# Optimization experiments

Measured on AMD Instinct MI355X. Metric: run time of the kernel, lower is better.

Reference implementation:

```python
import jax, jax.numpy as jnp
import numpy as np

B = 32768
IN_DIM = 256
HIDDEN = 256  # max(64, in_dim)
E = 8         # num_size_classes
K = 5         # num_depth_classes


def setup_inputs() -> dict:
    key = jax.random.key(0)
    ks = jax.random.split(key, 6)
    x = jax.random.normal(ks[0], (B, IN_DIM), dtype=jnp.float32)
    size_idx = jax.random.randint(ks[1], (B,), 0, E, dtype=jnp.int32)
    s1 = 1.0 / np.sqrt(IN_DIM)
    s2 = 1.0 / np.sqrt(HIDDEN)
    W1 = jax.random.uniform(ks[2], (E, IN_DIM, HIDDEN), jnp.float32, -s1, s1)
    b1 = jax.random.uniform(ks[3], (E, HIDDEN), jnp.float32, -s1, s1)
    W2 = jax.random.uniform(ks[4], (E, HIDDEN, K - 1), jnp.float32, -s2, s2)
    b2 = jax.random.uniform(ks[5], (E, K - 1), jnp.float32, -s2, s2)
    return {"x": x, "size_idx": size_idx, "W1": W1, "b1": b1, "W2": W2, "b2": b2}


def ordinal_logits_to_probs(logits):
    # logits: [B, K-1] cumulative ordinal logits -> [B, K] class probabilities
    q = jax.nn.sigmoid(logits)
    probs = jnp.concatenate(
        [1.0 - q[:, :1], q[:, :-1] - q[:, 1:], q[:, -1:]], axis=1)
    probs = jnp.clip(probs, 1e-8)
    return probs / jnp.clip(jnp.sum(probs, axis=1, keepdims=True), 1e-8)


def reference(x, size_idx, W1, b1, W2, b2):
    # Hard expert dispatch: each sample routed to expert[size_idx].
    # Equivalent to torch's boolean-mask loop (every row has a valid expert).
    # Compute all experts densely (grouped GEMM), then select per sample.
    h = jax.nn.relu(jnp.einsum('bi,eih->beh', x, W1) + b1)       # [B,E,H]
    logits_all = jnp.einsum('beh,ehk->bek', h, W2) + b2           # [B,E,K-1]
    idx = size_idx.astype(jnp.int32)[:, None, None]               # [B,1,1]
    logits = jnp.take_along_axis(logits_all, idx, axis=1)[:, 0]   # [B,K-1]
    probs = ordinal_logits_to_probs(logits)
    return logits, probs
```

## Files before the change

kernel.cpp:

```cpp
#include <hip/hip_runtime.h>
#include <stdint.h>
#include <math.h>

#define B_N   32768
#define INDIM 256
#define HID   256
#define NE    8
#define KM1   4
#define KCLS  5
#define BM    64
#define NBLK  ((B_N + NE * BM) / BM)

typedef __bf16 bf16x8 __attribute__((ext_vector_type(8)));
typedef float  f32x4  __attribute__((ext_vector_type(4)));
typedef unsigned short u16x8 __attribute__((ext_vector_type(8)));

__device__ __forceinline__ unsigned short f2bf(float f) {
    union { float f; unsigned u; } v; v.f = f;
    unsigned r = v.u + 0x7FFFu + ((v.u >> 16) & 1u);
    return (unsigned short)(r >> 16);
}
__device__ __forceinline__ float bf2f(unsigned short b) {
    union { unsigned u; float f; } v; v.u = ((unsigned)b) << 16;
    return v.f;
}
__device__ __forceinline__ int SWZ(int r, int c) {
    return c ^ ((r & 7) << 2) ^ ((r >> 3) & 3);
}

__global__ __launch_bounds__(256) void k_w1t(const float* __restrict__ W1,
                                             const int* __restrict__ sidx,
                                             unsigned short* __restrict__ w1p,
                                             int* __restrict__ part) {
    __shared__ float tile[64][65];
    __shared__ int wc[4][NE];
    int t    = threadIdx.x;
    int b    = blockIdx.x;
    int lane = t & 63;
    int wave = t >> 6;

    int i = b * 256 + t;
    int es = sidx[i];
    #pragma unroll
    for (int t2 = 0; t2 < NE; ++t2) {
        unsigned long long m = __ballot(es == t2);
        if (lane == t2) wc[wave][t2] = (int)__popcll(m);
    }

    int e  = b >> 4;
    int ti = (b >> 2) & 3;
    int th = b & 3;
    const float* src = W1 + (((size_t)e * INDIM) + (size_t)ti * 64) * HID + th * 64;
    int col = t & 63;
    int r0  = (t >> 6) * 16;
    #pragma unroll
    for (int rr = 0; rr < 16; ++rr)
        tile[r0 + rr][col] = src[(size_t)(r0 + rr) * HID + col];
    __syncthreads();

    if (t < NE) part[b * NE + t] = wc[0][t] + wc[1][t] + wc[2][t] + wc[3][t];

    int u = t >> 6;
    #pragma unroll
    for (int ks2 = 0; ks2 < 2; ++ks2) {
        int ks = ti * 2 + ks2;
        int nb = th * 4 + u;
        u16x8 v;
        #pragma unroll
        for (int j = 0; j < 8; ++j)
            v[j] = f2bf(tile[ks2 * 32 + (lane >> 4) * 8 + j][u * 16 + (lane & 15)]);
        *(u16x8*)&w1p[((((size_t)e * 8 + ks) * 16 + nb) * 64 + lane) * 8] = v;
    }
}

__global__ __launch_bounds__(256) void k_scatter(const int* __restrict__ sidx,
                                                 const int* __restrict__ part,
                                                 int* __restrict__ perm,
                                                 int* __restrict__ meta) {
    __shared__ int pp[128][NE];
    __shared__ int pre8[NE], tot8[NE];
    __shared__ int wc[4][NE];
    int t    = threadIdx.x;
    int b    = blockIdx.x;
    int lane = t & 63;
    int wave = t >> 6;

    if (t < 128) {
        #pragma unroll
        for (int e2 = 0; e2 < NE; ++e2) pp[t][e2] = part[t * NE + e2];
    }
    int i = b * 256 + t;
    int e = sidx[i];
    int posw = 0;
    #pragma unroll
    for (int t2 = 0; t2 < NE; ++t2) {
        unsigned long long m = __ballot(e == t2);
        if (e == t2) posw = (int)__popcll(m & ((1ull << lane) - 1ull));
        if (lane == t2) wc[wave][t2] = (int)__popcll(m);
    }
    __syncthreads();
    if (t < NE) {
        int s = 0, a = 0;
        for (int b2 = 0; b2 < 128; ++b2) {
            int v = pp[b2][t];
            if (b2 < b) s += v;
            a += v;
        }
        pre8[t] = s; tot8[t] = a;
        meta[t] = a;
    }
    __syncthreads();
    int off = 0;
    #pragma unroll
    for (int t2 = 0; t2 < NE; ++t2)
        off += (t2 < e) ? (((tot8[t2] + 63) >> 6) << 6) : 0;
    int wsum = 0;
    #pragma unroll
    for (int w2 = 0; w2 < 4; ++w2)
        wsum += (w2 < wave) ? wc[w2][e] : 0;
    perm[off + pre8[e] + wsum + posw] = i;
}

__global__ __launch_bounds__(256, 3) void k_main(
    const float* __restrict__ x,  const float* __restrict__ b1,
    const float* __restrict__ W2, const float* __restrict__ b2,
    const unsigned short* __restrict__ w1p,
    const int* __restrict__ perm, const int* __restrict__ meta,
    float* __restrict__ out)
{
    __shared__ unsigned short xs[BM * 256];
    __shared__ float w2s[1040];

    int base = blockIdx.x * BM;
    int e = 0, segstart = 0, segcnt = 0, acc_off = 0;
    #pragma unroll
    for (int t = 0; t < NE; ++t) {
        int c  = meta[t];
        int st = acc_off;
        acc_off += ((c + 63) >> 6) << 6;
        if (base >= st) { e = t; segstart = st; segcnt = c; }
    }
    if (base >= acc_off) return;
    int segend = segstart + segcnt;

    int tid  = threadIdx.x;
    int lane = tid & 63;
    int wave = tid >> 6;
    int r15  = lane & 15;
    int hi   = lane >> 4;

    {
        int row  = tid & 63;
        int q    = tid >> 6;
        int prow = base + row;
        int smp  = (prow < segend) ? perm[prow] : -1;
        const float* xr = x + (size_t)(smp < 0 ? 0 : smp) * INDIM + q * 64;
        #pragma unroll
        for (int cc = 0; cc < 8; ++cc) {
            int csw = SWZ(row, q * 8 + cc);
            u16x8 v = {0, 0, 0, 0, 0, 0, 0, 0};
            if (smp >= 0) {
                const f32x4* p4 = (const f32x4*)(xr + cc * 8);
                f32x4 a0 = p4[0], a1 = p4[1];
                v[0] = f2bf(a0[0]); v[1] = f2bf(a0[1]); v[2] = f2bf(a0[2]); v[3] = f2bf(a0[3]);
                v[4] = f2bf(a1[0]); v[5] = f2bf(a1[1]); v[6] = f2bf(a1[2]); v[7] = f2bf(a1[3]);
            }
            *(u16x8*)&xs[row * 256 + (csw << 3)] = v;
        }
    }
    {
        const float* w2e = W2 + (size_t)e * HID * KM1;
        f32x4 wv = *(const f32x4*)(w2e + (size_t)tid * 4);
        *(f32x4*)&w2s[tid * 4 + (tid >> 6) * 4] = wv;
    }
    __syncthreads();

    const unsigned short* w1pe = w1p + (size_t)e * (8 * 16 * 64 * 8);
    auto loadB = [&](int ks, int ni) -> bf16x8 {
        return *(const bf16x8*)&w1pe[(((ks * 16 + wave * 4 + ni) * 64) + lane) * 8];
    };

    f32x4 acc[4][4];
    #pragma unroll
    for (int mi = 0; mi < 4; ++mi)
        #pragma unroll
        for (int ni = 0; ni < 4; ++ni) {
            f32x4 z = {0.f, 0.f, 0.f, 0.f};
            acc[mi][ni] = z;
        }

    bf16x8 bcur[4];
    #pragma unroll
    for (int ni = 0; ni < 4; ++ni) bcur[ni] = loadB(0, ni);

    #pragma unroll
    for (int ks = 0; ks < 8; ++ks) {
        bf16x8 bnext[4];
        if (ks < 7) {
            #pragma unroll
            for (int ni = 0; ni < 4; ++ni) bnext[ni] = loadB(ks + 1, ni);
        }
        bf16x8 af[4];
        #pragma unroll
        for (int mi = 0; mi < 4; ++mi) {
            int r = mi * 16 + r15;
            af[mi] = *(const bf16x8*)&xs[r * 256 + (SWZ(r, ks * 4 + hi) << 3)];
        }
        #pragma unroll
        for (int mi = 0; mi < 4; ++mi)
            #pragma unroll
            for (int ni = 0; ni < 4; ++ni)
                acc[mi][ni] = __builtin_amdgcn_mfma_f32_16x16x32_bf16(
                    af[mi], bcur[ni], acc[mi][ni], 0, 0, 0);
        if (ks < 7) {
            #pragma unroll
            for (int ni = 0; ni < 4; ++ni) bcur[ni] = bnext[ni];
        }
    }
    __syncthreads();

    float b1v[4];
    #pragma unroll
    for (int ni = 0; ni < 4; ++ni)
        b1v[ni] = b1[e * HID + wave * 64 + ni * 16 + r15];
    #pragma unroll
    for (int mi = 0; mi < 4; ++mi) {
        #pragma unroll
        for (int ni = 0; ni < 4; ++ni) {
            int colg  = wave * 64 + ni * 16 + r15;
            int chunk = colg >> 3;
            #pragma unroll
            for (int j = 0; j < 4; ++j) {
                int rowg = mi * 16 + hi * 4 + j;
                float h = fmaxf(acc[mi][ni][j] + b1v[ni], 0.f);
                xs[rowg * 256 + (SWZ(rowg, chunk) << 3) + (colg & 7)] = f2bf(h);
            }
        }
    }
    __syncthreads();

    int row2 = tid >> 2;
    int q2   = tid & 3;
    f32x4 lac = {0.f, 0.f, 0.f, 0.f};
    #pragma unroll
    for (int s = 0; s < 8; ++s) {
        int c = q2 * 8 + s;
        u16x8 hv = *(const u16x8*)&xs[row2 * 256 + (SWZ(row2, c) << 3)];
        #pragma unroll
        for (int j = 0; j < 8; ++j) {
            int k = c * 8 + j;
            float hf = bf2f(hv[j]);
            const f32x4 wv = *(const f32x4*)&w2s[k * 4 + (k >> 6) * 4];
            lac[0] += hf * wv[0]; lac[1] += hf * wv[1];
            lac[2] += hf * wv[2]; lac[3] += hf * wv[3];
        }
    }
    #pragma unroll
    for (int c4 = 0; c4 < 4; ++c4) {
        lac[c4] += __shfl_xor(lac[c4], 1, 4);
        lac[c4] += __shfl_xor(lac[c4], 2, 4);
    }

    if (base + row2 < segend) {
        int smp = perm[base + row2];
        const float* b2e = b2 + e * KM1;
        float l0 = lac[0] + b2e[0], l1 = lac[1] + b2e[1];
        float l2 = lac[2] + b2e[2], l3 = lac[3] + b2e[3];
        float q0 = 1.f / (1.f + expf(-l0)), q1 = 1.f / (1.f + expf(-l1));
        float q2v = 1.f / (1.f + expf(-l2)), q3 = 1.f / (1.f + expf(-l3));
        float p0 = fmaxf(1.f - q0, 1e-8f), p1 = fmaxf(q0 - q1, 1e-8f);
        float p2 = fmaxf(q1 - q2v, 1e-8f), p3 = fmaxf(q2v - q3, 1e-8f);
        float p4 = fmaxf(q3, 1e-8f);
        float inv = 1.f / (p0 + p1 + p2 + p3 + p4);
        float myl = (q2 & 1) ? ((q2 & 2) ? l3 : l1) : ((q2 & 2) ? l2 : l0);
        float myp = (q2 & 1) ? ((q2 & 2) ? p3 : p1) : ((q2 & 2) ? p2 : p0);
        out[(size_t)smp * KM1 + q2] = myl;
        float* probs = out + (size_t)B_N * KM1;
        probs[(size_t)smp * KCLS + q2] = myp * inv;
        if (q2 == 3) probs[(size_t)smp * KCLS + 4] = p4 * inv;
    }
}

extern "C" void kernel_launch(void* const* d_in, const int* in_sizes, int n_in,
                              void* d_out, int out_size, void* d_ws, size_t ws_size,
                              hipStream_t stream) {
    const float* x   = (const float*)d_in[0];
    const int*   sid = (const int*)d_in[1];
    const float* W1  = (const float*)d_in[2];
    const float* b1  = (const float*)d_in[3];
    const float* W2  = (const float*)d_in[4];
    const float* b2  = (const float*)d_in[5];
    float* out = (float*)d_out;

    char* ws = (char*)d_ws;
    unsigned short* w1p = (unsigned short*)ws;
    int* perm = (int*)(ws + 1048576);
    int* part = (int*)(ws + 1048576 + 133120);
    int* meta = (int*)(ws + 1048576 + 133120 + 4096);

    k_w1t    <<<dim3(128),  dim3(256), 0, stream>>>(W1, sid, w1p, part);
    k_scatter<<<dim3(128),  dim3(256), 0, stream>>>(sid, part, perm, meta);
    k_main   <<<dim3(NBLK), dim3(256), 0, stream>>>(x, b1, W2, b2, w1p, perm, meta, out);
}
```

Baseline: 33.83 us.

## Halve row tile to 32, raise occupancy, hoist B prefetch above x staging

```diff
diff --git a/kernel.cpp b/kernel.cpp
--- a/kernel.cpp
+++ b/kernel.cpp
@@ -8,7 +8,7 @@
 #define NE    8
 #define KM1   4
 #define KCLS  5
-#define BM    64
+#define BM    32
 #define NBLK  ((B_N + NE * BM) / BM)
 
 typedef __bf16 bf16x8 __attribute__((ext_vector_type(8)));
@@ -24,9 +24,7 @@
     union { unsigned u; float f; } v; v.u = ((unsigned)b) << 16;
     return v.f;
 }
-__device__ __forceinline__ int SWZ(int r, int c) {
-    return c ^ ((r & 7) << 2) ^ ((r >> 3) & 3);
-}
+__device__ __forceinline__ int SWZ(int r, int c) { return c ^ (r & 7); }
 
 __global__ __launch_bounds__(256) void k_w1t(const float* __restrict__ W1,
                                              const int* __restrict__ sidx,
@@ -113,7 +111,7 @@
     int off = 0;
     #pragma unroll
     for (int t2 = 0; t2 < NE; ++t2)
-        off += (t2 < e) ? (((tot8[t2] + 63) >> 6) << 6) : 0;
+        off += (t2 < e) ? (((tot8[t2] + BM - 1) / BM) * BM) : 0;
     int wsum = 0;
     #pragma unroll
     for (int w2 = 0; w2 < 4; ++w2)
@@ -121,7 +119,7 @@
     perm[off + pre8[e] + wsum + posw] = i;
 }
 
-__global__ __launch_bounds__(256, 3) void k_main(
+__global__ __launch_bounds__(256, 4) void k_main(
     const float* __restrict__ x,  const float* __restrict__ b1,
     const float* __restrict__ W2, const float* __restrict__ b2,
     const unsigned short* __restrict__ w1p,
@@ -137,7 +135,7 @@
     for (int t = 0; t < NE; ++t) {
         int c  = meta[t];
         int st = acc_off;
-        acc_off += ((c + 63) >> 6) << 6;
+        acc_off += ((c + BM - 1) / BM) * BM;
         if (base >= st) { e = t; segstart = st; segcnt = c; }
     }
     if (base >= acc_off) return;
@@ -149,15 +147,22 @@
     int r15  = lane & 15;
     int hi   = lane >> 4;
 
+    const unsigned short* w1pe = w1p + (size_t)e * (8 * 16 * 64 * 8);
+    auto loadB = [&](int ks, int ni) -> bf16x8 {
+        return *(const bf16x8*)&w1pe[(((ks * 16 + wave * 4 + ni) * 64) + lane) * 8];
+    };
+    bf16x8 bcur[4];
+    #pragma unroll
+    for (int ni = 0; ni < 4; ++ni) bcur[ni] = loadB(0, ni);
+
+    int row = tid >> 3;
+    int q   = tid & 7;
+    int smp = (base + row < segend) ? perm[base + row] : -1;
     {
-        int row  = tid & 63;
-        int q    = tid >> 6;
-        int prow = base + row;
-        int smp  = (prow < segend) ? perm[prow] : -1;
-        const float* xr = x + (size_t)(smp < 0 ? 0 : smp) * INDIM + q * 64;
-        #pragma unroll
-        for (int cc = 0; cc < 8; ++cc) {
-            int csw = SWZ(row, q * 8 + cc);
+        const float* xr = x + (size_t)(smp < 0 ? 0 : smp) * INDIM + q * 32;
+        #pragma unroll
+        for (int cc = 0; cc < 4; ++cc) {
+            int csw = SWZ(row, q * 4 + cc);
             u16x8 v = {0, 0, 0, 0, 0, 0, 0, 0};
             if (smp >= 0) {
                 const f32x4* p4 = (const f32x4*)(xr + cc * 8);
@@ -175,23 +180,14 @@
     }
     __syncthreads();
 
-    const unsigned short* w1pe = w1p + (size_t)e * (8 * 16 * 64 * 8);
-    auto loadB = [&](int ks, int ni) -> bf16x8 {
-        return *(const bf16x8*)&w1pe[(((ks * 16 + wave * 4 + ni) * 64) + lane) * 8];
-    };
-
-    f32x4 acc[4][4];
-    #pragma unroll
-    for (int mi = 0; mi < 4; ++mi)
+    f32x4 acc[2][4];
+    #pragma unroll
+    for (int mi = 0; mi < 2; ++mi)
         #pragma unroll
         for (int ni = 0; ni < 4; ++ni) {
             f32x4 z = {0.f, 0.f, 0.f, 0.f};
             acc[mi][ni] = z;
         }
-
-    bf16x8 bcur[4];
-    #pragma unroll
-    for (int ni = 0; ni < 4; ++ni) bcur[ni] = loadB(0, ni);
 
     #pragma unroll
     for (int ks = 0; ks < 8; ++ks) {
@@ -200,14 +196,14 @@
             #pragma unroll
             for (int ni = 0; ni < 4; ++ni) bnext[ni] = loadB(ks + 1, ni);
         }
-        bf16x8 af[4];
-        #pragma unroll
-        for (int mi = 0; mi < 4; ++mi) {
+        bf16x8 af[2];
+        #pragma unroll
+        for (int mi = 0; mi < 2; ++mi) {
             int r = mi * 16 + r15;
             af[mi] = *(const bf16x8*)&xs[r * 256 + (SWZ(r, ks * 4 + hi) << 3)];
         }
         #pragma unroll
-        for (int mi = 0; mi < 4; ++mi)
+        for (int mi = 0; mi < 2; ++mi)
             #pragma unroll
             for (int ni = 0; ni < 4; ++ni)
                 acc[mi][ni] = __builtin_amdgcn_mfma_f32_16x16x32_bf16(
@@ -224,7 +220,7 @@
     for (int ni = 0; ni < 4; ++ni)
         b1v[ni] = b1[e * HID + wave * 64 + ni * 16 + r15];
     #pragma unroll
-    for (int mi = 0; mi < 4; ++mi) {
+    for (int mi = 0; mi < 2; ++mi) {
         #pragma unroll
         for (int ni = 0; ni < 4; ++ni) {
             int colg  = wave * 64 + ni * 16 + r15;
@@ -239,13 +235,11 @@
     }
     __syncthreads();
 
-    int row2 = tid >> 2;
-    int q2   = tid & 3;
     f32x4 lac = {0.f, 0.f, 0.f, 0.f};
     #pragma unroll
-    for (int s = 0; s < 8; ++s) {
-        int c = q2 * 8 + s;
-        u16x8 hv = *(const u16x8*)&xs[row2 * 256 + (SWZ(row2, c) << 3)];
+    for (int s = 0; s < 4; ++s) {
+        int c = q * 4 + ((s + q) & 3);
+        u16x8 hv = *(const u16x8*)&xs[row * 256 + (SWZ(row, c) << 3)];
         #pragma unroll
         for (int j = 0; j < 8; ++j) {
             int k = c * 8 + j;
@@ -257,12 +251,12 @@
     }
     #pragma unroll
     for (int c4 = 0; c4 < 4; ++c4) {
-        lac[c4] += __shfl_xor(lac[c4], 1, 4);
-        lac[c4] += __shfl_xor(lac[c4], 2, 4);
-    }
-
-    if (base + row2 < segend) {
-        int smp = perm[base + row2];
+        lac[c4] += __shfl_xor(lac[c4], 1, 8);
+        lac[c4] += __shfl_xor(lac[c4], 2, 8);
+        lac[c4] += __shfl_xor(lac[c4], 4, 8);
+    }
+
+    if (smp >= 0 && q < 5) {
         const float* b2e = b2 + e * KM1;
         float l0 = lac[0] + b2e[0], l1 = lac[1] + b2e[1];
         float l2 = lac[2] + b2e[2], l3 = lac[3] + b2e[3];
@@ -272,12 +266,15 @@
         float p2 = fmaxf(q1 - q2v, 1e-8f), p3 = fmaxf(q2v - q3, 1e-8f);
         float p4 = fmaxf(q3, 1e-8f);
         float inv = 1.f / (p0 + p1 + p2 + p3 + p4);
-        float myl = (q2 & 1) ? ((q2 & 2) ? l3 : l1) : ((q2 & 2) ? l2 : l0);
-        float myp = (q2 & 1) ? ((q2 & 2) ? p3 : p1) : ((q2 & 2) ? p2 : p0);
-        out[(size_t)smp * KM1 + q2] = myl;
         float* probs = out + (size_t)B_N * KM1;
-        probs[(size_t)smp * KCLS + q2] = myp * inv;
-        if (q2 == 3) probs[(size_t)smp * KCLS + 4] = p4 * inv;
+        if (q < 4) {
+            float myl = (q & 1) ? ((q & 2) ? l3 : l1) : ((q & 2) ? l2 : l0);
+            float myp = (q & 1) ? ((q & 2) ? p3 : p1) : ((q & 2) ? p2 : p0);
+            out[(size_t)smp * KM1 + q] = myl;
+            probs[(size_t)smp * KCLS + q] = myp * inv;
+        } else {
+            probs[(size_t)smp * KCLS + 4] = p4 * inv;
+        }
     }
 }
 
@@ -295,8 +292,8 @@
     char* ws = (char*)d_ws;
     unsigned short* w1p = (unsigned short*)ws;
     int* perm = (int*)(ws + 1048576);
-    int* part = (int*)(ws + 1048576 + 133120);
-    int* meta = (int*)(ws + 1048576 + 133120 + 4096);
+    int* part = (int*)(ws + 1048576 + 135168);
+    int* meta = (int*)(ws + 1048576 + 135168 + 4096);
 
     k_w1t    <<<dim3(128),  dim3(256), 0, stream>>>(W1, sid, w1p, part);
     k_scatter<<<dim3(128),  dim3(256), 0, stream>>>(sid, part, perm, meta);
```

Result: no change. 34.27 us (+1.3%).

## Fuse prep kernels, pre-scatter bf16 x into expert-bucketed buffer, DMA into LDS

Applied to the files above, without the earlier changes.

```diff
diff --git a/kernel.cpp b/kernel.cpp
--- a/kernel.cpp
+++ b/kernel.cpp
@@ -9,7 +9,9 @@
 #define KM1   4
 #define KCLS  5
 #define BM    64
-#define NBLK  ((B_N + NE * BM) / BM)
+#define CAP   8192
+#define TPE   (CAP / BM)
+#define NBLK  (NE * TPE)
 
 typedef __bf16 bf16x8 __attribute__((ext_vector_type(8)));
 typedef float  f32x4  __attribute__((ext_vector_type(4)));
@@ -24,124 +26,132 @@
     union { unsigned u; float f; } v; v.u = ((unsigned)b) << 16;
     return v.f;
 }
-__device__ __forceinline__ int SWZ(int r, int c) {
-    return c ^ ((r & 7) << 2) ^ ((r >> 3) & 3);
-}
-
-__global__ __launch_bounds__(256) void k_w1t(const float* __restrict__ W1,
-                                             const int* __restrict__ sidx,
-                                             unsigned short* __restrict__ w1p,
-                                             int* __restrict__ part) {
+__device__ __forceinline__ int SWZ(int r, int c) { return c ^ (r & 7); }
+
+__device__ __forceinline__ void gload_lds16(const void* g, void* l) {
+    __builtin_amdgcn_global_load_lds(
+        (__attribute__((address_space(1))) unsigned int*)(g),
+        (__attribute__((address_space(3))) unsigned int*)(l),
+        16, 0, 0);
+}
+
+__global__ __launch_bounds__(256) void k_prep(
+    const float* __restrict__ W1, const float* __restrict__ x,
+    const int* __restrict__ sidx,
+    unsigned short* __restrict__ w1p, unsigned short* __restrict__ xb,
+    int* __restrict__ perm, int* __restrict__ meta)
+{
     __shared__ float tile[64][65];
-    __shared__ int wc[4][NE];
+    __shared__ int wsum[4][NE];
+    __shared__ int gcnt[2][NE];
+    __shared__ int pcs[NE];
+    __shared__ int posbuf[128];
+
     int t    = threadIdx.x;
     int b    = blockIdx.x;
     int lane = t & 63;
     int wave = t >> 6;
 
-    int i = b * 256 + t;
-    int es = sidx[i];
-    #pragma unroll
-    for (int t2 = 0; t2 < NE; ++t2) {
-        unsigned long long m = __ballot(es == t2);
-        if (lane == t2) wc[wave][t2] = (int)__popcll(m);
-    }
-
-    int e  = b >> 4;
-    int ti = (b >> 2) & 3;
-    int th = b & 3;
-    const float* src = W1 + (((size_t)e * INDIM) + (size_t)ti * 64) * HID + th * 64;
-    int col = t & 63;
-    int r0  = (t >> 6) * 16;
-    #pragma unroll
-    for (int rr = 0; rr < 16; ++rr)
-        tile[r0 + rr][col] = src[(size_t)(r0 + rr) * HID + col];
-    __syncthreads();
-
-    if (t < NE) part[b * NE + t] = wc[0][t] + wc[1][t] + wc[2][t] + wc[3][t];
-
-    int u = t >> 6;
-    #pragma unroll
-    for (int ks2 = 0; ks2 < 2; ++ks2) {
-        int ks = ti * 2 + ks2;
-        int nb = th * 4 + u;
-        u16x8 v;
-        #pragma unroll
-        for (int j = 0; j < 8; ++j)
-            v[j] = f2bf(tile[ks2 * 32 + (lane >> 4) * 8 + j][u * 16 + (lane & 15)]);
-        *(u16x8*)&w1p[((((size_t)e * 8 + ks) * 16 + nb) * 64 + lane) * 8] = v;
-    }
-}
-
-__global__ __launch_bounds__(256) void k_scatter(const int* __restrict__ sidx,
-                                                 const int* __restrict__ part,
-                                                 int* __restrict__ perm,
-                                                 int* __restrict__ meta) {
-    __shared__ int pp[128][NE];
-    __shared__ int pre8[NE], tot8[NE];
-    __shared__ int wc[4][NE];
-    int t    = threadIdx.x;
-    int b    = blockIdx.x;
-    int lane = t & 63;
-    int wave = t >> 6;
-
+    if (b < 128) {
+        int e  = b >> 4, ti = (b >> 2) & 3, th = b & 3;
+        const float* src = W1 + (((size_t)e * INDIM) + (size_t)ti * 64) * HID + th * 64;
+        int col = t & 63, r0 = (t >> 6) * 16;
+        #pragma unroll
+        for (int rr = 0; rr < 16; ++rr)
+            tile[r0 + rr][col] = src[(size_t)(r0 + rr) * HID + col];
+    }
+
+    int cnt[NE] = {0, 0, 0, 0, 0, 0, 0, 0};
+    int nch = (b * 128) >> 6;
+    for (int j = wave; j < nch; j += 4) {
+        int v = sidx[j * 64 + lane];
+        #pragma unroll
+        for (int t2 = 0; t2 < NE; ++t2) {
+            unsigned long long m = __ballot(v == t2);
+            cnt[t2] += (int)__popcll(m);
+        }
+    }
+    if (lane == 0) {
+        #pragma unroll
+        for (int t2 = 0; t2 < NE; ++t2) wsum[wave][t2] = cnt[t2];
+    }
+    __syncthreads();
+    if (t < NE) pcs[t] = wsum[0][t] + wsum[1][t] + wsum[2][t] + wsum[3][t];
+
+    int e_own = 0, posw = 0;
     if (t < 128) {
-        #pragma unroll
-        for (int e2 = 0; e2 < NE; ++e2) pp[t][e2] = part[t * NE + e2];
-    }
-    int i = b * 256 + t;
-    int e = sidx[i];
-    int posw = 0;
-    #pragma unroll
-    for (int t2 = 0; t2 < NE; ++t2) {
-        unsigned long long m = __ballot(e == t2);
-        if (e == t2) posw = (int)__popcll(m & ((1ull << lane) - 1ull));
-        if (lane == t2) wc[wave][t2] = (int)__popcll(m);
-    }
-    __syncthreads();
-    if (t < NE) {
-        int s = 0, a = 0;
-        for (int b2 = 0; b2 < 128; ++b2) {
-            int v = pp[b2][t];
-            if (b2 < b) s += v;
-            a += v;
-        }
-        pre8[t] = s; tot8[t] = a;
-        meta[t] = a;
-    }
-    __syncthreads();
-    int off = 0;
-    #pragma unroll
-    for (int t2 = 0; t2 < NE; ++t2)
-        off += (t2 < e) ? (((tot8[t2] + 63) >> 6) << 6) : 0;
-    int wsum = 0;
-    #pragma unroll
-    for (int w2 = 0; w2 < 4; ++w2)
-        wsum += (w2 < wave) ? wc[w2][e] : 0;
-    perm[off + pre8[e] + wsum + posw] = i;
-}
-
-__global__ __launch_bounds__(256, 3) void k_main(
-    const float* __restrict__ x,  const float* __restrict__ b1,
-    const float* __restrict__ W2, const float* __restrict__ b2,
+        e_own = sidx[b * 128 + t];
+        #pragma unroll
+        for (int t2 = 0; t2 < NE; ++t2) {
+            unsigned long long m = __ballot(e_own == t2);
+            if (e_own == t2) posw = (int)__popcll(m & ((1ull << lane) - 1ull));
+            if (lane == t2) gcnt[wave][t2] = (int)__popcll(m);
+        }
+    }
+    __syncthreads();
+    if (t < 128) {
+        int grp  = (wave == 1) ? gcnt[0][e_own] : 0;
+        int rank = pcs[e_own] + grp + posw;
+        int pos  = e_own * CAP + rank;
+        posbuf[t] = pos;
+        perm[pos] = b * 128 + t;
+    }
+    if (b == 255 && t < NE) meta[t] = pcs[t] + gcnt[0][t] + gcnt[1][t];
+
+    if (b < 128) {
+        int e  = b >> 4, ti = (b >> 2) & 3, th = b & 3;
+        int u = t >> 6;
+        #pragma unroll
+        for (int ks2 = 0; ks2 < 2; ++ks2) {
+            int ks = ti * 2 + ks2, nb = th * 4 + u;
+            u16x8 v;
+            #pragma unroll
+            for (int j = 0; j < 8; ++j)
+                v[j] = f2bf(tile[ks2 * 32 + (lane >> 4) * 8 + j][u * 16 + (lane & 15)]);
+            *(u16x8*)&w1p[((((size_t)e * 8 + ks) * 16 + nb) * 64 + lane) * 8] = v;
+        }
+    }
+    __syncthreads();
+
+    {
+        int si  = t & 127, h = t >> 7;
+        int i   = b * 128 + si;
+        int pos = posbuf[si];
+        int r   = pos & (BM - 1);
+        const float* xr = x + (size_t)i * INDIM + h * 128;
+        unsigned short* dst = xb + (size_t)pos * 256;
+        #pragma unroll
+        for (int cc = 0; cc < 16; ++cc) {
+            int ch   = h * 16 + cc;
+            int slot = SWZ(r, ch);
+            f32x4 a0 = *(const f32x4*)(xr + cc * 8);
+            f32x4 a1 = *(const f32x4*)(xr + cc * 8 + 4);
+            u16x8 v;
+            v[0] = f2bf(a0[0]); v[1] = f2bf(a0[1]); v[2] = f2bf(a0[2]); v[3] = f2bf(a0[3]);
+            v[4] = f2bf(a1[0]); v[5] = f2bf(a1[1]); v[6] = f2bf(a1[2]); v[7] = f2bf(a1[3]);
+            *(u16x8*)&dst[slot * 8] = v;
+        }
+    }
+}
+
+__global__ __launch_bounds__(256, 4) void k_main(
+    const float* __restrict__ b1, const float* __restrict__ W2,
+    const float* __restrict__ b2,
     const unsigned short* __restrict__ w1p,
+    const unsigned short* __restrict__ xb,
     const int* __restrict__ perm, const int* __restrict__ meta,
     float* __restrict__ out)
 {
     __shared__ unsigned short xs[BM * 256];
     __shared__ float w2s[1040];
 
-    int base = blockIdx.x * BM;
-    int e = 0, segstart = 0, segcnt = 0, acc_off = 0;
-    #pragma unroll
-    for (int t = 0; t < NE; ++t) {
-        int c  = meta[t];
-        int st = acc_off;
-        acc_off += ((c + 63) >> 6) << 6;
-        if (base >= st) { e = t; segstart = st; segcnt = c; }
-    }
-    if (base >= acc_off) return;
-    int segend = segstart + segcnt;
+    int bid = (blockIdx.x & 7) * TPE + (blockIdx.x >> 3);
+    int e   = bid >> 7;
+    int tl  = bid & (TPE - 1);
+    int cnt = meta[e];
+    int rb  = tl * BM;
+    if (rb >= cnt) return;
+    int segc = cnt - rb;
 
     int tid  = threadIdx.x;
     int lane = tid & 63;
@@ -149,25 +159,19 @@
     int r15  = lane & 15;
     int hi   = lane >> 4;
 
-    {
-        int row  = tid & 63;
-        int q    = tid >> 6;
-        int prow = base + row;
-        int smp  = (prow < segend) ? perm[prow] : -1;
-        const float* xr = x + (size_t)(smp < 0 ? 0 : smp) * INDIM + q * 64;
-        #pragma unroll
-        for (int cc = 0; cc < 8; ++cc) {
-            int csw = SWZ(row, q * 8 + cc);
-            u16x8 v = {0, 0, 0, 0, 0, 0, 0, 0};
-            if (smp >= 0) {
-                const f32x4* p4 = (const f32x4*)(xr + cc * 8);
-                f32x4 a0 = p4[0], a1 = p4[1];
-                v[0] = f2bf(a0[0]); v[1] = f2bf(a0[1]); v[2] = f2bf(a0[2]); v[3] = f2bf(a0[3]);
-                v[4] = f2bf(a1[0]); v[5] = f2bf(a1[1]); v[6] = f2bf(a1[2]); v[7] = f2bf(a1[3]);
-            }
-            *(u16x8*)&xs[row * 256 + (csw << 3)] = v;
-        }
-    }
+    const unsigned short* xbt = xb + ((size_t)e * CAP + rb) * 256;
+    #pragma unroll
+    for (int it = 0; it < 8; ++it)
+        gload_lds16(xbt + ((size_t)it * 256 + tid) * 8, &xs[it * 2048 + wave * 512]);
+
+    const unsigned short* w1pe = w1p + (size_t)e * (8 * 16 * 64 * 8);
+    auto loadB = [&](int ks, int ni) -> bf16x8 {
+        return *(const bf16x8*)&w1pe[(((ks * 16 + wave * 4 + ni) * 64) + lane) * 8];
+    };
+    bf16x8 bcur[4];
+    #pragma unroll
+    for (int ni = 0; ni < 4; ++ni) bcur[ni] = loadB(0, ni);
+
     {
         const float* w2e = W2 + (size_t)e * HID * KM1;
         f32x4 wv = *(const f32x4*)(w2e + (size_t)tid * 4);
@@ -175,11 +179,6 @@
     }
     __syncthreads();
 
-    const unsigned short* w1pe = w1p + (size_t)e * (8 * 16 * 64 * 8);
-    auto loadB = [&](int ks, int ni) -> bf16x8 {
-        return *(const bf16x8*)&w1pe[(((ks * 16 + wave * 4 + ni) * 64) + lane) * 8];
-    };
-
     f32x4 acc[4][4];
     #pragma unroll
     for (int mi = 0; mi < 4; ++mi)
@@ -188,10 +187,6 @@
             f32x4 z = {0.f, 0.f, 0.f, 0.f};
             acc[mi][ni] = z;
         }
-
-    bf16x8 bcur[4];
-    #pragma unroll
-    for (int ni = 0; ni < 4; ++ni) bcur[ni] = loadB(0, ni);
 
     #pragma unroll
     for (int ks = 0; ks < 8; ++ks) {
@@ -239,13 +234,13 @@
     }
     __syncthreads();
 
-    int row2 = tid >> 2;
-    int q2   = tid & 3;
+    int row = tid >> 2;
+    int q   = tid & 3;
     f32x4 lac = {0.f, 0.f, 0.f, 0.f};
     #pragma unroll
     for (int s = 0; s < 8; ++s) {
-        int c = q2 * 8 + s;
-        u16x8 hv = *(const u16x8*)&xs[row2 * 256 + (SWZ(row2, c) << 3)];
+        int c = q * 8 + s;
+        u16x8 hv = *(const u16x8*)&xs[row * 256 + (SWZ(row, c) << 3)];
         #pragma unroll
         for (int j = 0; j < 8; ++j) {
             int k = c * 8 + j;
@@ -261,8 +256,8 @@
         lac[c4] += __shfl_xor(lac[c4], 2, 4);
     }
 
-    if (base + row2 < segend) {
-        int smp = perm[base + row2];
+    if (row < segc) {
+        int smp = perm[(size_t)e * CAP + rb + row];
         const float* b2e = b2 + e * KM1;
         float l0 = lac[0] + b2e[0], l1 = lac[1] + b2e[1];
         float l2 = lac[2] + b2e[2], l3 = lac[3] + b2e[3];
@@ -272,12 +267,12 @@
         float p2 = fmaxf(q1 - q2v, 1e-8f), p3 = fmaxf(q2v - q3, 1e-8f);
         float p4 = fmaxf(q3, 1e-8f);
         float inv = 1.f / (p0 + p1 + p2 + p3 + p4);
-        float myl = (q2 & 1) ? ((q2 & 2) ? l3 : l1) : ((q2 & 2) ? l2 : l0);
-        float myp = (q2 & 1) ? ((q2 & 2) ? p3 : p1) : ((q2 & 2) ? p2 : p0);
-        out[(size_t)smp * KM1 + q2] = myl;
+        float myl = (q & 1) ? ((q & 2) ? l3 : l1) : ((q & 2) ? l2 : l0);
+        float myp = (q & 1) ? ((q & 2) ? p3 : p1) : ((q & 2) ? p2 : p0);
+        out[(size_t)smp * KM1 + q] = myl;
         float* probs = out + (size_t)B_N * KM1;
-        probs[(size_t)smp * KCLS + q2] = myp * inv;
-        if (q2 == 3) probs[(size_t)smp * KCLS + 4] = p4 * inv;
+        probs[(size_t)smp * KCLS + q] = myp * inv;
+        if (q == 3) probs[(size_t)smp * KCLS + 4] = p4 * inv;
     }
 }
 
@@ -294,11 +289,10 @@
 
     char* ws = (char*)d_ws;
     unsigned short* w1p = (unsigned short*)ws;
-    int* perm = (int*)(ws + 1048576);
-    int* part = (int*)(ws + 1048576 + 133120);
-    int* meta = (int*)(ws + 1048576 + 133120 + 4096);
-
-    k_w1t    <<<dim3(128),  dim3(256), 0, stream>>>(W1, sid, w1p, part);
-    k_scatter<<<dim3(128),  dim3(256), 0, stream>>>(sid, part, perm, meta);
-    k_main   <<<dim3(NBLK), dim3(256), 0, stream>>>(x, b1, W2, b2, w1p, perm, meta, out);
-}
+    unsigned short* xb  = (unsigned short*)(ws + 1048576);
+    int* perm = (int*)(ws + 1048576 + 33554432);
+    int* meta = (int*)(ws + 1048576 + 33554432 + 262144);
+
+    k_prep<<<dim3(256),  dim3(256), 0, stream>>>(W1, x, sid, w1p, xb, perm, meta);
+    k_main<<<dim3(NBLK), dim3(256), 0, stream>>>(b1, W2, b2, w1p, xb, perm, meta, out);
+}
```

Measured after the change: 69.26 us. 2.05x slower.
